# Kernel tuning notes

Hardware: AMD Instinct MI355X
Metric: run time of the kernel (lower is better)

Reference implementation:

```python
import jax, jax.numpy as jnp
import numpy as np

N_NODES = 100000
N_FEATS = 2048
HIDDEN = 64
N_LABELS = 40
NNZ_FEAT = 2500000   # ~25 nonzero features per node
N_EDGES = 1600000    # avg degree 16 (directed COO entries)


def setup_inputs() -> dict:
    key = jax.random.key(0)
    ks = jax.random.split(key, 10)

    # sparse feature matrix [N_NODES, N_FEATS] in COO form
    f_rows = jax.random.randint(ks[0], (NNZ_FEAT,), 0, N_NODES)
    f_cols = jax.random.randint(ks[1], (NNZ_FEAT,), 0, N_FEATS)
    feature_indices = jnp.stack([f_rows, f_cols]).astype(jnp.int64)
    feature_values = jax.random.uniform(ks[2], (NNZ_FEAT,), dtype=jnp.float32)

    # random graph edges + self loops, then D^-1/2 (A+I) D^-1/2 normalization
    e_rows = jax.random.randint(ks[3], (N_EDGES,), 0, N_NODES)
    e_cols = jax.random.randint(ks[4], (N_EDGES,), 0, N_NODES)
    loops = jnp.arange(N_NODES)
    rows = jnp.concatenate([e_rows, loops])
    cols = jnp.concatenate([e_cols, loops])
    deg = jax.ops.segment_sum(jnp.ones_like(rows, dtype=jnp.float32), rows,
                              num_segments=N_NODES)
    deg = deg + jax.ops.segment_sum(jnp.ones_like(cols, dtype=jnp.float32), cols,
                                    num_segments=N_NODES)
    d_inv_sqrt = jax.lax.rsqrt(jnp.maximum(deg * 0.5, 1.0))
    edge_indices = jnp.stack([rows, cols]).astype(jnp.int64)
    edge_weights = d_inv_sqrt[rows] * d_inv_sqrt[cols]

    # xavier-uniform weights, uniform(-1/sqrt(out), 1/sqrt(out)) biases
    lim1 = np.sqrt(6.0 / (N_FEATS + HIDDEN))
    W1 = jax.random.uniform(ks[5], (N_FEATS, HIDDEN), jnp.float32, -lim1, lim1)
    b1 = jax.random.uniform(ks[6], (HIDDEN,), jnp.float32,
                            -1.0 / np.sqrt(HIDDEN), 1.0 / np.sqrt(HIDDEN))
    lim2 = np.sqrt(6.0 / (HIDDEN + N_LABELS))
    W2 = jax.random.uniform(ks[7], (HIDDEN, N_LABELS), jnp.float32, -lim2, lim2)
    b2 = jax.random.uniform(ks[8], (N_LABELS,), jnp.float32,
                            -1.0 / np.sqrt(N_LABELS), 1.0 / np.sqrt(N_LABELS))

    return {"feature_indices": feature_indices, "feature_values": feature_values,
            "edge_indices": edge_indices, "edge_weights": edge_weights,
            "W1": W1, "b1": b1, "W2": W2, "b2": b2}


def _spmm(rows, cols, vals, dense):
    # (sparse [N, M]) @ (dense [M, D]) -> [N, D]
    return jax.ops.segment_sum(vals[:, None] * dense[cols], rows,
                               num_segments=N_NODES)


def reference(feature_indices, feature_values, edge_indices, edge_weights,
              W1, b1, W2, b2):
    f_rows, f_cols = feature_indices
    e_rows, e_cols = edge_indices

    # layer 1: sparse feature SpMM + bias
    h = _spmm(f_rows, f_cols, feature_values, W1) + b1        # [N, HIDDEN]
    # propagate with normalized adjacency, relu (dropout is identity in eval)
    h = jax.nn.relu(_spmm(e_rows, e_cols, edge_weights, h))   # [N, HIDDEN]
    # layer 2: dense linear
    z = h @ W2 + b2                                           # [N, N_LABELS]
    # propagate again
    z = _spmm(e_rows, e_cols, edge_weights, z)                # [N, N_LABELS]
    return jax.nn.log_softmax(z, axis=1)
```

## Files before the change

### kernel.cpp

```cpp
#include <hip/hip_runtime.h>
#include <hip/hip_bf16.h>


#define HID 64
#define LAB 40
#define RSH 8
#define RPB (1 << RSH)
#define KMAX 1024
#define TILE_A 6144
#define EPT 6
#define CAPB 6912

typedef __attribute__((ext_vector_type(8))) short short8;
typedef __attribute__((ext_vector_type(4))) float f32x4;

__device__ __forceinline__ float loadF(const void* p, size_t i, int bf16) {
    if (bf16) return __bfloat162float(((const __hip_bfloat16*)p)[i]);
    return ((const float*)p)[i];
}

__device__ __forceinline__ int loadI(const void* p, size_t i, int i64) {
    if (i64) return (int)(((const long long*)p)[i]);
    return ((const int*)p)[i];
}

__device__ __forceinline__ float bflo(unsigned v) { return __uint_as_float(v << 16); }
__device__ __forceinline__ float bfhi(unsigned v) { return __uint_as_float(v & 0xFFFF0000u); }
__device__ __forceinline__ unsigned bfr16(float x) {
    unsigned u = __float_as_uint(x);
    return (u + 0x7FFFu + ((u >> 16) & 1u)) >> 16;
}
__device__ __forceinline__ unsigned bfpack(float lo, float hi) {
    return bfr16(lo) | (bfr16(hi) << 16);
}

__device__ __forceinline__ unsigned fp8pack4(float a, float b, float c, float d) {
    int r = __builtin_amdgcn_cvt_pk_fp8_f32(a, b, 0, false);
    r = __builtin_amdgcn_cvt_pk_fp8_f32(c, d, r, true);
    return (unsigned)r;
}

__device__ __forceinline__ void ntload(const int2* P, int idx, int* c, float* w) {
    long long raw = __builtin_nontemporal_load((const long long*)P + idx);
    *c = (int)(unsigned)(raw & 0xFFFFFFFFll);
    *w = __int_as_float((int)(raw >> 32));
}

__device__ __forceinline__ short8 cvt8(uint2 u) {
    short8 r;
    r[0] = (short)bfr16(__builtin_amdgcn_cvt_f32_fp8((int)u.x, 0));
    r[1] = (short)bfr16(__builtin_amdgcn_cvt_f32_fp8((int)u.x, 1));
    r[2] = (short)bfr16(__builtin_amdgcn_cvt_f32_fp8((int)u.x, 2));
    r[3] = (short)bfr16(__builtin_amdgcn_cvt_f32_fp8((int)u.x, 3));
    r[4] = (short)bfr16(__builtin_amdgcn_cvt_f32_fp8((int)u.y, 0));
    r[5] = (short)bfr16(__builtin_amdgcn_cvt_f32_fp8((int)u.y, 1));
    r[6] = (short)bfr16(__builtin_amdgcn_cvt_f32_fp8((int)u.y, 2));
    r[7] = (short)bfr16(__builtin_amdgcn_cvt_f32_fp8((int)u.y, 3));
    return r;
}

__global__ __launch_bounds__(512)
void prep_kernel(const void* W1, const void* b1p, const void* fidxp,
                 const void* W2, uint2* w1q, uint4* w2f, int* cntB,
                 int* flags, int ne) {
    __shared__ int sf[2];
    const int t = threadIdx.x;
    if (t == 0) {
        const unsigned short* u = (const unsigned short*)b1p;
        int bf16 = 1;
        for (int i = 0; i < 64; i += 2)
            if ((unsigned short)(u[i] & 0x7FFF) >= 0x3E80) { bf16 = 0; break; }
        const int* ip = (const int*)fidxp;
        int i64 = 1;
        for (int i = 1; i < 128; i += 2)
            if (ip[i] != 0) { i64 = 0; break; }
        sf[0] = bf16; sf[1] = i64;
        if (blockIdx.x == 0) {
            flags[0] = bf16; flags[1] = i64; flags[2] = 0; flags[3] = 0;
        }
    }
    __syncthreads();
    const int bf16 = sf[0];
    int i = blockIdx.x * 512 + t;
    if (i < ne) {
        float f0 = loadF(W1, (size_t)4 * i,     bf16);
        float f1 = loadF(W1, (size_t)4 * i + 1, bf16);
        float f2 = loadF(W1, (size_t)4 * i + 2, bf16);
        float f3 = loadF(W1, (size_t)4 * i + 3, bf16);
        w1q[i] = make_uint2(bfpack(f0, f1), bfpack(f2, f3));
    }
    if (blockIdx.x == 0) {
        cntB[t] = 0;
        cntB[t + 512] = 0;
        if (t < 384) {
            int tt   = t >> 7;
            int kh   = (t >> 6) & 1;
            int lane = t & 63;
            int col  = tt * 16 + (lane & 15);
            int kb   = kh * 32 + (lane >> 4) * 8;
            unsigned d[4];
#pragma unroll
            for (int q = 0; q < 8; q += 2) {
                float v0 = (col < LAB) ? loadF(W2, (size_t)(kb + q) * LAB + col, bf16) : 0.f;
                float v1 = (col < LAB) ? loadF(W2, (size_t)(kb + q + 1) * LAB + col, bf16) : 0.f;
                d[q >> 1] = bfpack(v0, v1);
            }
            w2f[(tt * 2 + kh) * 64 + lane] = make_uint4(d[0], d[1], d[2], d[3]);
        }
    }
}

__global__ __launch_bounds__(1024)
void histB_kernel(const void* fidx, const void* eidx, int* cntB, int* cntPB,
                  const int* flags, int nnz, int nE, int N, int nblk) {
    __shared__ int lh[KMAX];
    lh[threadIdx.x] = 0;
    __syncthreads();
    const int i64 = flags[1];
    const int nT = nnz + nE;
    const int base = blockIdx.x * TILE_A;
#pragma unroll
    for (int k = 0; k < EPT; k++) {
        int i = base + k * 1024 + threadIdx.x;
        if (i < nT) {
            int grow = (i < nnz) ? loadI(fidx, (size_t)i, i64)
                                 : N + loadI(eidx, (size_t)(i - nnz), i64);
            atomicAdd(&lh[grow >> RSH], 1);
        }
    }
    __syncthreads();
    {
        int c = lh[threadIdx.x];
        cntPB[(size_t)threadIdx.x * nblk + blockIdx.x] = c;
        if (c) atomicAdd(&cntB[threadIdx.x], c);
    }
}

__global__ __launch_bounds__(1024)
void scanPB_kernel(int* cntPB, const int* cntB, int* bqstart, int nblk, int K) {
    __shared__ int sb[KMAX];
    __shared__ int se[KMAX];
    __shared__ int s[1024];
    const int b = blockIdx.x;
    const int t = threadIdx.x;
    int c0 = (t < K) ? cntB[t] : 0;
    sb[t] = c0;
    __syncthreads();
    for (int off = 1; off < KMAX; off <<= 1) {
        int v = (t >= off) ? sb[t - off] : 0;
        __syncthreads();
        sb[t] += v;
        __syncthreads();
    }
    se[t] = sb[t] - c0;
    if (t == b) bqstart[b] = se[t];
    __syncthreads();
    const int bqs = se[b];
    int x = (t < nblk) ? cntPB[(size_t)b * nblk + t] : 0;
    s[t] = x;
    __syncthreads();
    for (int off = 1; off < 1024; off <<= 1) {
        int v = (t >= off) ? s[t - off] : 0;
        __syncthreads();
        s[t] += v;
        __syncthreads();
    }
    if (t < nblk) cntPB[(size_t)b * nblk + t] = bqs + s[t] - x;
}

__global__ __launch_bounds__(1024)
void bucketA_kernel(const void* fidx, const void* fval,
                    const void* eidx, const void* ew,
                    const int* flags, const int* cntPB, int2* Q,
                    int nnz, int nE, int N, int nblk) {
    __shared__ int2 stage[TILE_A];
    __shared__ int hist[KMAX];
    __shared__ int lofs[KMAX + 1];
    __shared__ int delta[KMAX];
    const int i64 = flags[1], bf16 = flags[0];
    const int nT = nnz + nE;
    const int base = blockIdx.x * TILE_A;
    const int t = threadIdx.x;
    hist[t] = 0;
    __syncthreads();

    int key[EPT]; float val[EPT]; int bk[EPT]; int rk[EPT];
#pragma unroll
    for (int k = 0; k < EPT; k++) {
        int i = base + k * 1024 + t;
        bk[k] = -1; rk[k] = 0; key[k] = 0; val[k] = 0.f;
        if (i < nT) {
            int grow, c; float v;
            if (i < nnz) {
                grow = loadI(fidx, (size_t)i, i64);
                c    = loadI(fidx, (size_t)nnz + i, i64);
                v    = loadF(fval, (size_t)i, bf16);
            } else {
                int j = i - nnz;
                grow = N + loadI(eidx, (size_t)j, i64);
                c    = loadI(eidx, (size_t)nE + j, i64);
                v    = loadF(ew, (size_t)j, bf16);
            }
            int b = grow >> RSH;
            bk[k]  = b;
            key[k] = ((grow & (RPB - 1)) << 17) | c;
            val[k] = v;
            rk[k]  = atomicAdd(&hist[b], 1);
        }
    }
    __syncthreads();

    int cnt = hist[t];
    delta[t] = cnt;
    __syncthreads();
    for (int off2 = 1; off2 < KMAX; off2 <<= 1) {
        int v2 = (t >= off2) ? delta[t - off2] : 0;
        __syncthreads();
        delta[t] += v2;
        __syncthreads();
    }
    {
        int incl = delta[t];
        int excl = incl - cnt;
        lofs[t] = excl;
        if (t == KMAX - 1) lofs[KMAX] = incl;
        delta[t] = cntPB[(size_t)t * nblk + blockIdx.x] - excl;
    }
    __syncthreads();

#pragma unroll
    for (int k = 0; k < EPT; k++) {
        if (bk[k] >= 0)
            stage[lofs[bk[k]] + rk[k]] = make_int2(key[k], __float_as_int(val[k]));
    }
    __syncthreads();

    const int total = min(TILE_A, nT - base);
    for (int p = t; p < total; p += 1024) {
        int b = 0;
#pragma unroll
        for (int step = KMAX / 2; step; step >>= 1)
            if (lofs[b + step] <= p) b += step;
        Q[delta[b] + p] = stage[p];
    }
}

__global__ __launch_bounds__(1024)
void bucketB_kernel(const int2* Q, const int* bqstart, int* rp,
                    int2* P, int nT, int K) {
    __shared__ int2 stg[CAPB];
    __shared__ int lh[RPB];
    __shared__ int s[RPB];
    __shared__ int lstart[RPB];
    const int b = blockIdx.x;
    const int t = threadIdx.x;
    const int start = bqstart[b];
    const int end = (b == K - 1) ? nT : bqstart[b + 1];
    const int cnt = end - start;
    if (t < RPB) lh[t] = 0;
    __syncthreads();
    for (int i = start + t; i < end; i += 1024)
        atomicAdd(&lh[((unsigned)Q[i].x) >> 17], 1);
    __syncthreads();
    int x = (t < RPB) ? lh[t] : 0;
    if (t < RPB) s[t] = x;
    __syncthreads();
    for (int off = 1; off < RPB; off <<= 1) {
        int v = (t >= off && t < RPB) ? s[t - off] : 0;
        __syncthreads();
        if (t < RPB) s[t] += v;
        __syncthreads();
    }
    if (t < RPB) {
        int excl = s[t] - x;
        rp[(b << RSH) + t] = start + excl;
        lstart[t] = excl;
        lh[t] = 0;
    }
    __syncthreads();
    if (cnt <= CAPB) {
        for (int i = start + t; i < end; i += 1024) {
            int2 el = Q[i];
            int lr = ((unsigned)el.x) >> 17;
            int rank = atomicAdd(&lh[lr], 1);
            stg[lstart[lr] + rank] = make_int2(el.x & 0x1FFFF, el.y);
        }
        __syncthreads();
        for (int p = t; p < cnt; p += 1024)
            P[start + p] = stg[p];
    } else {
        for (int i = start + t; i < end; i += 1024) {
            int2 el = Q[i];
            int lr = ((unsigned)el.x) >> 17;
            int rank = atomicAdd(&lh[lr], 1);
            P[start + lstart[lr] + rank] = make_int2(el.x & 0x1FFFF, el.y);
        }
    }
}

__global__ void gather_feat_kernel(const int* rp, const int2* P,
                                   const uint2* w1q, const void* b1,
                                   unsigned* hF8, const int* flags, int N) {
    int bf16 = flags[0];
    int wave = (blockIdx.x * blockDim.x + threadIdx.x) >> 6;
    int lane = threadIdx.x & 63;
    int g = lane >> 4, gl = lane & 15;
    int row = 4 * wave + g;
    int s = 0, e = 0;
    if (row < N) { s = rp[row]; e = rp[row + 1]; }
    float a0 = loadF(b1, (size_t)4 * gl,     bf16);
    float a1 = loadF(b1, (size_t)4 * gl + 1, bf16);
    float a2 = loadF(b1, (size_t)4 * gl + 2, bf16);
    float a3 = loadF(b1, (size_t)4 * gl + 3, bf16);
    const int sb = g << 4;
    int cl = 0; float vl = 0.f;
    if (s + gl < e) ntload(P, s + gl, &cl, &vl);
    for (int base = s; base < e; base += 16) {
        int ncl = 0; float nvl = 0.f;
        int nidx = base + 16 + gl;
        if (nidx < e) ntload(P, nidx, &ncl, &nvl);
        int cnt = min(16, e - base);
        if (cnt == 16) {
            int   cc[16]; float vv[16];
#pragma unroll
            for (int j = 0; j < 16; j++) {
                cc[j] = __shfl(cl, sb + j);
                vv[j] = __shfl(vl, sb + j);
            }
            uint2 uu[16];
#pragma unroll
            for (int j = 0; j < 16; j++) uu[j] = w1q[cc[j] * 16 + gl];
#pragma unroll
            for (int j = 0; j < 16; j++) {
                a0 += vv[j] * bflo(uu[j].x); a1 += vv[j] * bfhi(uu[j].x);
                a2 += vv[j] * bflo(uu[j].y); a3 += vv[j] * bfhi(uu[j].y);
            }
        } else {
            for (int j = 0; j < cnt; j++) {
                int   c = __shfl(cl, sb + j);
                float v = __shfl(vl, sb + j);
                uint2 u = w1q[c * 16 + gl];
                a0 += v * bflo(u.x); a1 += v * bfhi(u.x);
                a2 += v * bflo(u.y); a3 += v * bfhi(u.y);
            }
        }
        cl = ncl; vl = nvl;
    }
    if (row < N) hF8[row * 16 + gl] = fp8pack4(a0, a1, a2, a3);
}

__global__ void gather_edge_h2_kernel(const int* rp, const int2* P,
                                      const unsigned* hF8, unsigned* h2F8,
                                      int N) {
    int wave = (blockIdx.x * blockDim.x + threadIdx.x) >> 6;
    int lane = threadIdx.x & 63;
    int g = lane >> 4, gl = lane & 15;
    int row = 4 * wave + g;
    int s = 0, e = 0;
    if (row < N) { s = rp[N + row]; e = rp[N + row + 1]; }
    float a0 = 0.f, a1 = 0.f, a2 = 0.f, a3 = 0.f;
    const int sb = g << 4;
    int cl = 0; float wl = 0.f;
    if (s + gl < e) ntload(P, s + gl, &cl, &wl);
    for (int base = s; base < e; base += 16) {
        int ncl = 0; float nwl = 0.f;
        int nidx = base + 16 + gl;
        if (nidx < e) ntload(P, nidx, &ncl, &nwl);
        int cnt = min(16, e - base);
        int j = 0;
        for (; j + 8 <= cnt; j += 8) {
            int   c0 = __shfl(cl, sb + j),     c1 = __shfl(cl, sb + j + 1);
            int   c2 = __shfl(cl, sb + j + 2), c3 = __shfl(cl, sb + j + 3);
            int   c4 = __shfl(cl, sb + j + 4), c5 = __shfl(cl, sb + j + 5);
            int   c6 = __shfl(cl, sb + j + 6), c7 = __shfl(cl, sb + j + 7);
            float w0 = __shfl(wl, sb + j),     w1 = __shfl(wl, sb + j + 1);
            float w2 = __shfl(wl, sb + j + 2), w3 = __shfl(wl, sb + j + 3);
            float w4 = __shfl(wl, sb + j + 4), w5 = __shfl(wl, sb + j + 5);
            float w6 = __shfl(wl, sb + j + 6), w7 = __shfl(wl, sb + j + 7);
            int u0 = (int)hF8[c0 * 16 + gl];
            int u1 = (int)hF8[c1 * 16 + gl];
            int u2 = (int)hF8[c2 * 16 + gl];
            int u3 = (int)hF8[c3 * 16 + gl];
            int u4 = (int)hF8[c4 * 16 + gl];
            int u5 = (int)hF8[c5 * 16 + gl];
            int u6 = (int)hF8[c6 * 16 + gl];
            int u7 = (int)hF8[c7 * 16 + gl];
            a0 += w0 * __builtin_amdgcn_cvt_f32_fp8(u0, 0);
            a1 += w0 * __builtin_amdgcn_cvt_f32_fp8(u0, 1);
            a2 += w0 * __builtin_amdgcn_cvt_f32_fp8(u0, 2);
            a3 += w0 * __builtin_amdgcn_cvt_f32_fp8(u0, 3);
            a0 += w1 * __builtin_amdgcn_cvt_f32_fp8(u1, 0);
            a1 += w1 * __builtin_amdgcn_cvt_f32_fp8(u1, 1);
            a2 += w1 * __builtin_amdgcn_cvt_f32_fp8(u1, 2);
            a3 += w1 * __builtin_amdgcn_cvt_f32_fp8(u1, 3);
            a0 += w2 * __builtin_amdgcn_cvt_f32_fp8(u2, 0);
            a1 += w2 * __builtin_amdgcn_cvt_f32_fp8(u2, 1);
            a2 += w2 * __builtin_amdgcn_cvt_f32_fp8(u2, 2);
            a3 += w2 * __builtin_amdgcn_cvt_f32_fp8(u2, 3);
            a0 += w3 * __builtin_amdgcn_cvt_f32_fp8(u3, 0);
            a1 += w3 * __builtin_amdgcn_cvt_f32_fp8(u3, 1);
            a2 += w3 * __builtin_amdgcn_cvt_f32_fp8(u3, 2);
            a3 += w3 * __builtin_amdgcn_cvt_f32_fp8(u3, 3);
            a0 += w4 * __builtin_amdgcn_cvt_f32_fp8(u4, 0);
            a1 += w4 * __builtin_amdgcn_cvt_f32_fp8(u4, 1);
            a2 += w4 * __builtin_amdgcn_cvt_f32_fp8(u4, 2);
            a3 += w4 * __builtin_amdgcn_cvt_f32_fp8(u4, 3);
            a0 += w5 * __builtin_amdgcn_cvt_f32_fp8(u5, 0);
            a1 += w5 * __builtin_amdgcn_cvt_f32_fp8(u5, 1);
            a2 += w5 * __builtin_amdgcn_cvt_f32_fp8(u5, 2);
            a3 += w5 * __builtin_amdgcn_cvt_f32_fp8(u5, 3);
            a0 += w6 * __builtin_amdgcn_cvt_f32_fp8(u6, 0);
            a1 += w6 * __builtin_amdgcn_cvt_f32_fp8(u6, 1);
            a2 += w6 * __builtin_amdgcn_cvt_f32_fp8(u6, 2);
            a3 += w6 * __builtin_amdgcn_cvt_f32_fp8(u6, 3);
            a0 += w7 * __builtin_amdgcn_cvt_f32_fp8(u7, 0);
            a1 += w7 * __builtin_amdgcn_cvt_f32_fp8(u7, 1);
            a2 += w7 * __builtin_amdgcn_cvt_f32_fp8(u7, 2);
            a3 += w7 * __builtin_amdgcn_cvt_f32_fp8(u7, 3);
        }
        for (; j < cnt; j++) {
            int   c = __shfl(cl, sb + j);
            float w = __shfl(wl, sb + j);
            int u = (int)hF8[c * 16 + gl];
            a0 += w * __builtin_amdgcn_cvt_f32_fp8(u, 0);
            a1 += w * __builtin_amdgcn_cvt_f32_fp8(u, 1);
            a2 += w * __builtin_amdgcn_cvt_f32_fp8(u, 2);
            a3 += w * __builtin_amdgcn_cvt_f32_fp8(u, 3);
        }
        cl = ncl; wl = nwl;
    }
    if (row < N)
        h2F8[row * 16 + gl] = fp8pack4(fmaxf(a0, 0.f), fmaxf(a1, 0.f),
                                       fmaxf(a2, 0.f), fmaxf(a3, 0.f));
}

__global__ void dense_mfma_kernel(const unsigned* h2F8, const uint4* w2f,
                                  const void* b2, unsigned char* zb,
                                  const int* flags, int N) {
    int bf16 = flags[0];
    int wid  = (int)((blockIdx.x * blockDim.x + threadIdx.x) >> 6);
    int lane = threadIdx.x & 63;
    int ntiles = (N + 15) >> 4;
    if (wid >= ntiles) return;
    const int g = lane >> 4;
    const int fr = lane & 15;

    int arow = wid * 16 + fr;
    const uint2* hrow = (const uint2*)(h2F8 + (size_t)arow * 16);
    short8 af0 = cvt8(hrow[g]);
    short8 af1 = cvt8(hrow[4 + g]);

    f32x4 acc[3];
#pragma unroll
    for (int t = 0; t < 3; t++) {
        int col = t * 16 + fr;
        float bias = (col < LAB) ? loadF(b2, (size_t)col, bf16) : 0.f;
        acc[t][0] = bias; acc[t][1] = bias; acc[t][2] = bias; acc[t][3] = bias;
        uint4 b0 = w2f[(t * 2 + 0) * 64 + lane];
        uint4 b1 = w2f[(t * 2 + 1) * 64 + lane];
        acc[t] = __builtin_amdgcn_mfma_f32_16x16x32_bf16(
            af0, *(short8*)&b0, acc[t], 0, 0, 0);
        acc[t] = __builtin_amdgcn_mfma_f32_16x16x32_bf16(
            af1, *(short8*)&b1, acc[t], 0, 0, 0);
    }

#pragma unroll
    for (int t = 0; t < 3; t++) {
        int col = t * 16 + fr;
        if (col < LAB) {
#pragma unroll
            for (int q = 0; q < 4; q++) {
                int orow = wid * 16 + g * 4 + q;
                if (orow < N) {
                    int pk = __builtin_amdgcn_cvt_pk_fp8_f32(acc[t][q], acc[t][q], 0, false);
                    zb[(size_t)orow * LAB + col] = (unsigned char)(pk & 0xFF);
                }
            }
        }
    }
}

__global__ void gather_edge_lsm_kernel(const int* rp, const int2* P,
                                       const unsigned* zF8, void* out,
                                       const int* flags, int N) {
    int bf16 = flags[0];
    int wave = (blockIdx.x * blockDim.x + threadIdx.x) >> 6;
    int lane = threadIdx.x & 63;
    int g = lane >> 4, gl = lane & 15;
    int row = 4 * wave + g;
    int s = 0, e = 0;
    if (row < N) { s = rp[N + row]; e = rp[N + row + 1]; }
    float a0 = 0.f, a1 = 0.f, a2 = 0.f, a3 = 0.f;
    const int sb = g << 4;
    const int act = (gl < 10);
    int cl = 0; float wl = 0.f;
    if (s + gl < e) ntload(P, s + gl, &cl, &wl);
    for (int base = s; base < e; base += 16) {
        int ncl = 0; float nwl = 0.f;
        int nidx = base + 16 + gl;
        if (nidx < e) ntload(P, nidx, &ncl, &nwl);
        int cnt = min(16, e - base);
        int j = 0;
        for (; j + 8 <= cnt; j += 8) {
            int   c0 = __shfl(cl, sb + j),     c1 = __shfl(cl, sb + j + 1);
            int   c2 = __shfl(cl, sb + j + 2), c3 = __shfl(cl, sb + j + 3);
            int   c4 = __shfl(cl, sb + j + 4), c5 = __shfl(cl, sb + j + 5);
            int   c6 = __shfl(cl, sb + j + 6), c7 = __shfl(cl, sb + j + 7);
            float w0 = __shfl(wl, sb + j),     w1 = __shfl(wl, sb + j + 1);
            float w2 = __shfl(wl, sb + j + 2), w3 = __shfl(wl, sb + j + 3);
            float w4 = __shfl(wl, sb + j + 4), w5 = __shfl(wl, sb + j + 5);
            float w6 = __shfl(wl, sb + j + 6), w7 = __shfl(wl, sb + j + 7);
            if (act) {
                int u0 = (int)zF8[c0 * 10 + gl];
                int u1 = (int)zF8[c1 * 10 + gl];
                int u2 = (int)zF8[c2 * 10 + gl];
                int u3 = (int)zF8[c3 * 10 + gl];
                int u4 = (int)zF8[c4 * 10 + gl];
                int u5 = (int)zF8[c5 * 10 + gl];
                int u6 = (int)zF8[c6 * 10 + gl];
                int u7 = (int)zF8[c7 * 10 + gl];
                a0 += w0 * __builtin_amdgcn_cvt_f32_fp8(u0, 0);
                a1 += w0 * __builtin_amdgcn_cvt_f32_fp8(u0, 1);
                a2 += w0 * __builtin_amdgcn_cvt_f32_fp8(u0, 2);
                a3 += w0 * __builtin_amdgcn_cvt_f32_fp8(u0, 3);
                a0 += w1 * __builtin_amdgcn_cvt_f32_fp8(u1, 0);
                a1 += w1 * __builtin_amdgcn_cvt_f32_fp8(u1, 1);
                a2 += w1 * __builtin_amdgcn_cvt_f32_fp8(u1, 2);
                a3 += w1 * __builtin_amdgcn_cvt_f32_fp8(u1, 3);
                a0 += w2 * __builtin_amdgcn_cvt_f32_fp8(u2, 0);
                a1 += w2 * __builtin_amdgcn_cvt_f32_fp8(u2, 1);
                a2 += w2 * __builtin_amdgcn_cvt_f32_fp8(u2, 2);
                a3 += w2 * __builtin_amdgcn_cvt_f32_fp8(u2, 3);
                a0 += w3 * __builtin_amdgcn_cvt_f32_fp8(u3, 0);
                a1 += w3 * __builtin_amdgcn_cvt_f32_fp8(u3, 1);
                a2 += w3 * __builtin_amdgcn_cvt_f32_fp8(u3, 2);
                a3 += w3 * __builtin_amdgcn_cvt_f32_fp8(u3, 3);
                a0 += w4 * __builtin_amdgcn_cvt_f32_fp8(u4, 0);
                a1 += w4 * __builtin_amdgcn_cvt_f32_fp8(u4, 1);
                a2 += w4 * __builtin_amdgcn_cvt_f32_fp8(u4, 2);
                a3 += w4 * __builtin_amdgcn_cvt_f32_fp8(u4, 3);
                a0 += w5 * __builtin_amdgcn_cvt_f32_fp8(u5, 0);
                a1 += w5 * __builtin_amdgcn_cvt_f32_fp8(u5, 1);
                a2 += w5 * __builtin_amdgcn_cvt_f32_fp8(u5, 2);
                a3 += w5 * __builtin_amdgcn_cvt_f32_fp8(u5, 3);
                a0 += w6 * __builtin_amdgcn_cvt_f32_fp8(u6, 0);
                a1 += w6 * __builtin_amdgcn_cvt_f32_fp8(u6, 1);
                a2 += w6 * __builtin_amdgcn_cvt_f32_fp8(u6, 2);
                a3 += w6 * __builtin_amdgcn_cvt_f32_fp8(u6, 3);
                a0 += w7 * __builtin_amdgcn_cvt_f32_fp8(u7, 0);
                a1 += w7 * __builtin_amdgcn_cvt_f32_fp8(u7, 1);
                a2 += w7 * __builtin_amdgcn_cvt_f32_fp8(u7, 2);
                a3 += w7 * __builtin_amdgcn_cvt_f32_fp8(u7, 3);
            }
        }
        for (; j < cnt; j++) {
            int   c = __shfl(cl, sb + j);
            float w = __shfl(wl, sb + j);
            if (act) {
                int u = (int)zF8[c * 10 + gl];
                a0 += w * __builtin_amdgcn_cvt_f32_fp8(u, 0);
                a1 += w * __builtin_amdgcn_cvt_f32_fp8(u, 1);
                a2 += w * __builtin_amdgcn_cvt_f32_fp8(u, 2);
                a3 += w * __builtin_amdgcn_cvt_f32_fp8(u, 3);
            }
        }
        cl = ncl; wl = nwl;
    }
    float m = act ? fmaxf(fmaxf(a0, a1), fmaxf(a2, a3)) : -INFINITY;
#pragma unroll
    for (int off = 8; off; off >>= 1) m = fmaxf(m, __shfl_xor(m, off));
    float es = act ? (__expf(a0 - m) + __expf(a1 - m) + __expf(a2 - m) + __expf(a3 - m)) : 0.f;
#pragma unroll
    for (int off = 8; off; off >>= 1) es += __shfl_xor(es, off);
    float lse = m + __logf(es);
    if (act && row < N) {
        float o0 = a0 - lse, o1 = a1 - lse, o2 = a2 - lse, o3 = a3 - lse;
        if (bf16) {
            ((uint2*)out)[(size_t)row * 10 + gl] =
                make_uint2(bfpack(o0, o1), bfpack(o2, o3));
        } else {
            float4 v = make_float4(o0, o1, o2, o3);
            ((float4*)out)[(size_t)row * 10 + gl] = v;
        }
    }
}

extern "C" void kernel_launch(void* const* d_in, const int* in_sizes, int n_in,
                              void* d_out, int out_size, void* d_ws, size_t ws_size,
                              hipStream_t stream) {
    const void* fidx = d_in[0];
    const void* fval = d_in[1];
    const void* eidx = d_in[2];
    const void* ew   = d_in[3];
    const void* W1   = d_in[4];
    const void* b1   = d_in[5];
    const void* W2   = d_in[6];
    const void* b2   = d_in[7];

    const int nnz = in_sizes[1];
    const int nW1 = in_sizes[4];
    const int nE  = in_sizes[3];
    const int N   = out_size / LAB;
    const int M   = 2 * N;
    const int nT  = nnz + nE;
    const int K   = (M + RPB - 1) >> RSH;
    const int NBLK = (nT + TILE_A - 1) / TILE_A;

    auto align256 = [](size_t x) { return (x + 255) & ~(size_t)255; };
    char* ws = (char*)d_ws;
    size_t off = 0;
    int*   flags   = (int*)(ws + off);   off += 256;
    char*  front   = ws + off;
    unsigned* hF8  = (unsigned*)front;
    unsigned* h2F8 = hF8 + (size_t)N * 16;
    unsigned char* zb = (unsigned char*)(h2F8 + (size_t)N * 16);
    size_t frontBytes = (size_t)N * (64 + 64 + 40);
    size_t qBytes     = (size_t)nT * 8;
    off += align256(frontBytes > qBytes ? frontBytes : qBytes);
    int2*  P       = (int2*)(ws + off);  off += align256((size_t)nT * 8);
    int*   rp      = (int*)(ws + off);   off += align256(((size_t)KMAX << RSH) * 4 + 16);
    uint2* w1q     = (uint2*)(ws + off); off += align256((size_t)nW1 * 2);
    uint4* w2f     = (uint4*)(ws + off); off += align256((size_t)384 * 16);
    int*   cntB    = (int*)(ws + off);   off += KMAX * 4;
    int*   bqstart = (int*)(ws + off);   off += KMAX * 4;
    int*   cntPB   = (int*)(ws + off);   off += align256((size_t)KMAX * NBLK * 4);
    int2*  Q       = (int2*)front;

    prep_kernel<<<(nW1 / 4 + 511) / 512, 512, 0, stream>>>(
        W1, b1, fidx, W2, w1q, w2f, cntB, flags, nW1 / 4);

    histB_kernel<<<NBLK, 1024, 0, stream>>>(fidx, eidx, cntB, cntPB,
                                            flags, nnz, nE, N, NBLK);

    scanPB_kernel<<<K, 1024, 0, stream>>>(cntPB, cntB, bqstart, NBLK, K);

    bucketA_kernel<<<NBLK, 1024, 0, stream>>>(fidx, fval, eidx, ew, flags,
                                              cntPB, Q, nnz, nE, N, NBLK);

    bucketB_kernel<<<K, 1024, 0, stream>>>(Q, bqstart, rp, P, nT, K);

    int nwaves = (N + 3) / 4;
    int gblocks = (int)(((size_t)nwaves * 64 + 255) / 256);
    gather_feat_kernel<<<gblocks, 256, 0, stream>>>(rp, P, w1q, b1, hF8, flags, N);

    gather_edge_h2_kernel<<<gblocks, 256, 0, stream>>>(rp, P, hF8, h2F8, N);

    int ntiles = (N + 15) / 16;
    int dblocks = (int)(((size_t)ntiles * 64 + 255) / 256);
    dense_mfma_kernel<<<dblocks, 256, 0, stream>>>(h2F8, w2f, b2, zb, flags, N);

    gather_edge_lsm_kernel<<<gblocks, 256, 0, stream>>>(rp, P, (const unsigned*)zb,
                                                        d_out, flags, N);
}
```

Baseline: 278.9 us.

## Remap feature gather to 8 lanes per row with 16-byte loads

New measurement: 269.0 us (median of 2 runs). 3.5% less time.

```diff
diff --git a/kernel.cpp b/kernel.cpp
--- a/kernel.cpp
+++ b/kernel.cpp
@@ -304,49 +304,60 @@
     int bf16 = flags[0];
     int wave = (blockIdx.x * blockDim.x + threadIdx.x) >> 6;
     int lane = threadIdx.x & 63;
-    int g = lane >> 4, gl = lane & 15;
-    int row = 4 * wave + g;
+    int g = lane >> 3, gl = lane & 7;
+    int row = 8 * wave + g;
     int s = 0, e = 0;
     if (row < N) { s = rp[row]; e = rp[row + 1]; }
-    float a0 = loadF(b1, (size_t)4 * gl,     bf16);
-    float a1 = loadF(b1, (size_t)4 * gl + 1, bf16);
-    float a2 = loadF(b1, (size_t)4 * gl + 2, bf16);
-    float a3 = loadF(b1, (size_t)4 * gl + 3, bf16);
-    const int sb = g << 4;
+    const uint4* w1q4 = (const uint4*)w1q;
+    float a0 = loadF(b1, (size_t)8 * gl,     bf16);
+    float a1 = loadF(b1, (size_t)8 * gl + 1, bf16);
+    float a2 = loadF(b1, (size_t)8 * gl + 2, bf16);
+    float a3 = loadF(b1, (size_t)8 * gl + 3, bf16);
+    float a4 = loadF(b1, (size_t)8 * gl + 4, bf16);
+    float a5 = loadF(b1, (size_t)8 * gl + 5, bf16);
+    float a6 = loadF(b1, (size_t)8 * gl + 6, bf16);
+    float a7 = loadF(b1, (size_t)8 * gl + 7, bf16);
+    const int sb = g << 3;
     int cl = 0; float vl = 0.f;
     if (s + gl < e) ntload(P, s + gl, &cl, &vl);
-    for (int base = s; base < e; base += 16) {
+    for (int base = s; base < e; base += 8) {
         int ncl = 0; float nvl = 0.f;
-        int nidx = base + 16 + gl;
+        int nidx = base + 8 + gl;
         if (nidx < e) ntload(P, nidx, &ncl, &nvl);
-        int cnt = min(16, e - base);
-        if (cnt == 16) {
-            int   cc[16]; float vv[16];
-#pragma unroll
-            for (int j = 0; j < 16; j++) {
+        int cnt = min(8, e - base);
+        if (cnt == 8) {
+            int   cc[8]; float vv[8];
+#pragma unroll
+            for (int j = 0; j < 8; j++) {
                 cc[j] = __shfl(cl, sb + j);
                 vv[j] = __shfl(vl, sb + j);
             }
-            uint2 uu[16];
-#pragma unroll
-            for (int j = 0; j < 16; j++) uu[j] = w1q[cc[j] * 16 + gl];
-#pragma unroll
-            for (int j = 0; j < 16; j++) {
+            uint4 uu[8];
+#pragma unroll
+            for (int j = 0; j < 8; j++) uu[j] = w1q4[cc[j] * 8 + gl];
+#pragma unroll
+            for (int j = 0; j < 8; j++) {
                 a0 += vv[j] * bflo(uu[j].x); a1 += vv[j] * bfhi(uu[j].x);
                 a2 += vv[j] * bflo(uu[j].y); a3 += vv[j] * bfhi(uu[j].y);
+                a4 += vv[j] * bflo(uu[j].z); a5 += vv[j] * bfhi(uu[j].z);
+                a6 += vv[j] * bflo(uu[j].w); a7 += vv[j] * bfhi(uu[j].w);
             }
         } else {
             for (int j = 0; j < cnt; j++) {
                 int   c = __shfl(cl, sb + j);
                 float v = __shfl(vl, sb + j);
-                uint2 u = w1q[c * 16 + gl];
+                uint4 u = w1q4[c * 8 + gl];
                 a0 += v * bflo(u.x); a1 += v * bfhi(u.x);
                 a2 += v * bflo(u.y); a3 += v * bfhi(u.y);
+                a4 += v * bflo(u.z); a5 += v * bfhi(u.z);
+                a6 += v * bflo(u.w); a7 += v * bfhi(u.w);
             }
         }
         cl = ncl; vl = nvl;
     }
-    if (row < N) hF8[row * 16 + gl] = fp8pack4(a0, a1, a2, a3);
+    if (row < N)
+        ((uint2*)hF8)[(size_t)row * 8 + gl] =
+            make_uint2(fp8pack4(a0, a1, a2, a3), fp8pack4(a4, a5, a6, a7));
 }
 
 __global__ void gather_edge_h2_kernel(const int* rp, const int2* P,
@@ -501,24 +512,16 @@
         if (nidx < e) ntload(P, nidx, &ncl, &nwl);
         int cnt = min(16, e - base);
         int j = 0;
-        for (; j + 8 <= cnt; j += 8) {
+        for (; j + 4 <= cnt; j += 4) {
             int   c0 = __shfl(cl, sb + j),     c1 = __shfl(cl, sb + j + 1);
             int   c2 = __shfl(cl, sb + j + 2), c3 = __shfl(cl, sb + j + 3);
-            int   c4 = __shfl(cl, sb + j + 4), c5 = __shfl(cl, sb + j + 5);
-            int   c6 = __shfl(cl, sb + j + 6), c7 = __shfl(cl, sb + j + 7);
             float w0 = __shfl(wl, sb + j),     w1 = __shfl(wl, sb + j + 1);
             float w2 = __shfl(wl, sb + j + 2), w3 = __shfl(wl, sb + j + 3);
-            float w4 = __shfl(wl, sb + j + 4), w5 = __shfl(wl, sb + j + 5);
-            float w6 = __shfl(wl, sb + j + 6), w7 = __shfl(wl, sb + j + 7);
             if (act) {
                 int u0 = (int)zF8[c0 * 10 + gl];
                 int u1 = (int)zF8[c1 * 10 + gl];
                 int u2 = (int)zF8[c2 * 10 + gl];
                 int u3 = (int)zF8[c3 * 10 + gl];
-                int u4 = (int)zF8[c4 * 10 + gl];
-                int u5 = (int)zF8[c5 * 10 + gl];
-                int u6 = (int)zF8[c6 * 10 + gl];
-                int u7 = (int)zF8[c7 * 10 + gl];
                 a0 += w0 * __builtin_amdgcn_cvt_f32_fp8(u0, 0);
                 a1 += w0 * __builtin_amdgcn_cvt_f32_fp8(u0, 1);
                 a2 += w0 * __builtin_amdgcn_cvt_f32_fp8(u0, 2);
@@ -535,22 +538,6 @@
                 a1 += w3 * __builtin_amdgcn_cvt_f32_fp8(u3, 1);
                 a2 += w3 * __builtin_amdgcn_cvt_f32_fp8(u3, 2);
                 a3 += w3 * __builtin_amdgcn_cvt_f32_fp8(u3, 3);
-                a0 += w4 * __builtin_amdgcn_cvt_f32_fp8(u4, 0);
-                a1 += w4 * __builtin_amdgcn_cvt_f32_fp8(u4, 1);
-                a2 += w4 * __builtin_amdgcn_cvt_f32_fp8(u4, 2);
-                a3 += w4 * __builtin_amdgcn_cvt_f32_fp8(u4, 3);
-                a0 += w5 * __builtin_amdgcn_cvt_f32_fp8(u5, 0);
-                a1 += w5 * __builtin_amdgcn_cvt_f32_fp8(u5, 1);
-                a2 += w5 * __builtin_amdgcn_cvt_f32_fp8(u5, 2);
-                a3 += w5 * __builtin_amdgcn_cvt_f32_fp8(u5, 3);
-                a0 += w6 * __builtin_amdgcn_cvt_f32_fp8(u6, 0);
-                a1 += w6 * __builtin_amdgcn_cvt_f32_fp8(u6, 1);
-                a2 += w6 * __builtin_amdgcn_cvt_f32_fp8(u6, 2);
-                a3 += w6 * __builtin_amdgcn_cvt_f32_fp8(u6, 3);
-                a0 += w7 * __builtin_amdgcn_cvt_f32_fp8(u7, 0);
-                a1 += w7 * __builtin_amdgcn_cvt_f32_fp8(u7, 1);
-                a2 += w7 * __builtin_amdgcn_cvt_f32_fp8(u7, 2);
-                a3 += w7 * __builtin_amdgcn_cvt_f32_fp8(u7, 3);
             }
         }
         for (; j < cnt; j++) {
@@ -639,10 +626,12 @@
 
     bucketB_kernel<<<K, 1024, 0, stream>>>(Q, bqstart, rp, P, nT, K);
 
+    int fw = (N + 7) / 8;
+    int fblocks = (int)(((size_t)fw * 64 + 255) / 256);
+    gather_feat_kernel<<<fblocks, 256, 0, stream>>>(rp, P, w1q, b1, hF8, flags, N);
+
     int nwaves = (N + 3) / 4;
     int gblocks = (int)(((size_t)nwaves * 64 + 255) / 256);
-    gather_feat_kernel<<<gblocks, 256, 0, stream>>>(rp, P, w1q, b1, hF8, flags, N);
-
     gather_edge_h2_kernel<<<gblocks, 256, 0, stream>>>(rp, P, hF8, h2F8, N);
 
     int ntiles = (N + 15) / 16;
```
